# Performance work log

Measured on AMD Instinct MI355X. Metric: run time of the kernel, lower is better.

The kernel has to match this reference:

```python
import jax, jax.numpy as jnp
import numpy as np

D_MODEL = 1024
HIDDEN = 4096
N_EXPERTS = 8
LB_COEF = 0.01
B, N = 2, 2048


def setup_inputs() -> dict:
    key = jax.random.key(0)
    k_x, k_g, k_w1, k_w2 = jax.random.split(key, 4)
    s = 0.02
    return {
        "x": jax.random.normal(k_x, (B, N, D_MODEL), dtype=jnp.float32),
        "gate_w": jax.random.normal(k_g, (N_EXPERTS, D_MODEL), dtype=jnp.float32) * s,
        "w1": jax.random.normal(k_w1, (N_EXPERTS, HIDDEN, D_MODEL), dtype=jnp.float32) * s,  # torch Linear weight [out,in]
        "b1": jnp.zeros((N_EXPERTS, HIDDEN), dtype=jnp.float32),
        "w2": jax.random.normal(k_w2, (N_EXPERTS, D_MODEL, HIDDEN), dtype=jnp.float32) * s,
        "b2": jnp.zeros((N_EXPERTS, D_MODEL), dtype=jnp.float32),
    }


def reference(x, gate_w, w1, b1, w2, b2):
    # gate logits: Linear(d_model, E, bias=False)
    logits = jnp.einsum('bnd,ed->bne', x, gate_w)
    probs = jax.nn.softmax(logits, axis=-1)            # router_prob
    gate_scores = jnp.max(probs, axis=-1)              # top-1 prob [B,N]
    sel = jnp.argmax(probs, axis=-1)                   # selected expert [B,N]

    # load-balance aux loss
    onehot = jax.nn.one_hot(sel, N_EXPERTS, dtype=x.dtype)
    f = onehot.mean(axis=(0, 1))                       # fraction of tokens per expert
    P = probs.mean(axis=(0, 1))                        # mean router prob per expert
    aux_loss = LB_COEF * N_EXPERTS * jnp.sum(f * P)

    # dispatch: loop over fixed small expert count (structurally distinct weights)
    out = jnp.zeros_like(x)
    for e in range(N_EXPERTS):
        h = jax.nn.gelu(jnp.einsum('bnd,hd->bnh', x, w1[e]) + b1[e], approximate=False)
        y = jnp.einsum('bnh,dh->bnd', h, w2[e]) + b2[e]
        out = out + jnp.where((sel == e)[..., None], gate_scores[..., None] * y, jnp.zeros((), x.dtype))
    return out, aux_loss
```

## Files before the change

### kernel.cpp

```cpp
#include <hip/hip_runtime.h>
#include <math.h>

#define T_TOK 4096
#define DM 1024
#define HID 4096
#define NEXP 8
#define MAXT 39

typedef unsigned short u16;
typedef __attribute__((ext_vector_type(8))) short short8;
typedef __attribute__((ext_vector_type(4))) float f32x4;

__device__ __forceinline__ u16 f2bf(float f){
  unsigned u = __float_as_uint(f);
  u += 0x7FFF + ((u >> 16) & 1);
  return (u16)(u >> 16);
}

#define GATE_OFF   0u
#define CNT_OFF    16384u
#define LIST_OFF   16512u
#define PROBS_OFF  147584u
#define XB_OFF     278656u
#define H_OFF      8667264u
#define W1B_OFF    42221696u
#define PART_OFF   W1B_OFF
#define W2B_OFF    109330560u

__device__ __forceinline__ void glds16(const void* g, void* l){
  __builtin_amdgcn_global_load_lds((const __attribute__((address_space(1))) void*)g,
                                   (__attribute__((address_space(3))) void*)l, 16, 0, 0);
}

__global__ void zero_cnt_kernel(int* cnt){
  if (threadIdx.x < NEXP) cnt[threadIdx.x] = 0;
}

__global__ __launch_bounds__(256) void cvt_kernel(const float* __restrict__ src,
                                                  u16* __restrict__ dst,
                                                  size_t n8){
  size_t stride = (size_t)gridDim.x * 256;
  for (size_t i = (size_t)blockIdx.x * 256 + threadIdx.x; i < n8; i += stride){
    const float4* s = (const float4*)src + i * 2;
    float4 a = s[0], c = s[1];
    uint4 p;
    p.x = (unsigned)f2bf(a.x) | ((unsigned)f2bf(a.y) << 16);
    p.y = (unsigned)f2bf(a.z) | ((unsigned)f2bf(a.w) << 16);
    p.z = (unsigned)f2bf(c.x) | ((unsigned)f2bf(c.y) << 16);
    p.w = (unsigned)f2bf(c.z) | ((unsigned)f2bf(c.w) << 16);
    ((uint4*)dst)[i] = p;
  }
}

__global__ __launch_bounds__(256) void gate_kernel(
    const float* __restrict__ x, const float* __restrict__ gw,
    float* __restrict__ gateo, int* __restrict__ cnt, int* __restrict__ list,
    float* __restrict__ probs, u16* __restrict__ xb)
{
  int tid = threadIdx.x;
  int lane = tid & 63;
  int w = tid >> 6;
  int t = blockIdx.x * 4 + w;

  const float4* x4 = (const float4*)(x + (size_t)t * DM);
  const float4* g4 = (const float4*)gw;

  float acc[8] = {0,0,0,0,0,0,0,0};
  #pragma unroll
  for (int i = 0; i < 4; i++){
    int p = i * 64 + lane;
    float4 xv = x4[p];
    ushort4 pk;
    pk.x = f2bf(xv.x); pk.y = f2bf(xv.y); pk.z = f2bf(xv.z); pk.w = f2bf(xv.w);
    *(ushort4*)&xb[(size_t)t * DM + (size_t)p * 4] = pk;
    #pragma unroll
    for (int e = 0; e < NEXP; e++){
      float4 gv = g4[e * 256 + p];
      acc[e] += xv.x * gv.x + xv.y * gv.y + xv.z * gv.z + xv.w * gv.w;
    }
  }
  #pragma unroll
  for (int e = 0; e < NEXP; e++){
    #pragma unroll
    for (int off = 32; off; off >>= 1)
      acc[e] += __shfl_xor(acc[e], off);
  }
  if (lane == 0){
    float mx = acc[0];
    #pragma unroll
    for (int e = 1; e < NEXP; e++) mx = fmaxf(mx, acc[e]);
    float p[8]; float s = 0.f;
    #pragma unroll
    for (int e = 0; e < NEXP; e++){ p[e] = expf(acc[e] - mx); s += p[e]; }
    float inv = 1.f / s;
    int be = 0; float bp = p[0];
    #pragma unroll
    for (int e = 1; e < NEXP; e++){ if (p[e] > bp){ bp = p[e]; be = e; } }
    #pragma unroll
    for (int e = 0; e < NEXP; e++) probs[(size_t)t * 8 + e] = p[e] * inv;
    gateo[t] = bp * inv;
    int pos = atomicAdd(&cnt[be], 1);
    list[be * T_TOK + pos] = t;
  }
}

__global__ __launch_bounds__(256) void aux_kernel(
    const float* __restrict__ probs, const int* __restrict__ cnt,
    float* __restrict__ aux_out)
{
  __shared__ float sm[256 * 8];
  int tid = threadIdx.x;
  float s[8] = {0,0,0,0,0,0,0,0};
  for (int i = 0; i < 16; i++){
    int t = i * 256 + tid;
    #pragma unroll
    for (int e = 0; e < 8; e++) s[e] += probs[(size_t)t * 8 + e];
  }
  #pragma unroll
  for (int e = 0; e < 8; e++) sm[tid * 8 + e] = s[e];
  __syncthreads();
  for (int st = 128; st; st >>= 1){
    if (tid < st){
      #pragma unroll
      for (int e = 0; e < 8; e++) sm[tid * 8 + e] += sm[(tid + st) * 8 + e];
    }
    __syncthreads();
  }
  if (tid == 0){
    float a = 0.f;
    #pragma unroll
    for (int e = 0; e < 8; e++){
      float f = (float)cnt[e] / (float)T_TOK;
      float P = sm[e] / (float)T_TOK;
      a += f * P;
    }
    aux_out[0] = 0.01f * (float)NEXP * a;
  }
}

template<int ASTR, int BSTR, int NTOT, int NT, int KS, bool PHASE2>
__global__ __launch_bounds__(256, 3) void ffn_gemm(
    const u16*  __restrict__ Aall,
    const u16*  __restrict__ Bb,
    const float* __restrict__ bias,
    const int*  __restrict__ cnt,
    const int*  __restrict__ list,
    u16*  __restrict__ hOut,
    float* __restrict__ pOut)
{
  int bid = blockIdx.x;
  int nt = bid % NT;
  int r1 = bid / NT;
  int t  = r1 % MAXT;
  int sk = r1 / MAXT;

  int e = -1, mt = 0, accT = 0;
  #pragma unroll
  for (int i = 0; i < NEXP; i++){
    int nti = (cnt[i] + 127) >> 7;
    if (e < 0 && t < accT + nti){ e = i; mt = t - accT; }
    accT += nti;
  }
  if (e < 0) return;
  int ne = cnt[e];
  int m0 = mt * 128;
  const int* lst = list + e * T_TOK;
  int n0 = nt * 128;
  int koff = sk * (KS * 64);

  __shared__ u16 As[8192];
  __shared__ u16 Bs[8192];

  int tid  = threadIdx.x;
  int lane = tid & 63;
  int w    = tid >> 6;
  int wm = w >> 1, wn = w & 1;
  int fr = lane & 15, fq = lane >> 4;

  const u16* aS[4]; const u16* bS[4]; int dst[4];
  #pragma unroll
  for (int i = 0; i < 4; i++){
    int seg = w * 4 + i;
    int r   = seg * 8 + (lane >> 3);
    int g   = (lane & 7) ^ (r & 7);
    int mrow = m0 + r; if (mrow > ne - 1) mrow = ne - 1;
    aS[i] = Aall + (size_t)lst[mrow] * ASTR + koff + g * 8;
    bS[i] = Bb + (size_t)e * NTOT * BSTR + (size_t)(n0 + r) * BSTR + koff + g * 8;
    dst[i] = seg * 512;
  }

  f32x4 acc[4][4];
  #pragma unroll
  for (int m = 0; m < 4; m++)
    #pragma unroll
    for (int n = 0; n < 4; n++)
      acc[m][n] = (f32x4){0.f, 0.f, 0.f, 0.f};

  for (int ks = 0; ks < KS; ++ks){
    if (ks) __syncthreads();
    size_t ko = (size_t)ks * 64;
    #pragma unroll
    for (int i = 0; i < 4; i++) glds16(aS[i] + ko, &As[dst[i]]);
    #pragma unroll
    for (int i = 0; i < 4; i++) glds16(bS[i] + ko, &Bs[dst[i]]);
    __syncthreads();
    #pragma unroll
    for (int kc = 0; kc < 2; kc++){
      short8 afr[4], bfr[4];
      #pragma unroll
      for (int m = 0; m < 4; m++){
        int row  = wm * 64 + m * 16 + fr;
        int slot = (kc * 4 + fq) ^ (row & 7);
        afr[m] = *(const short8*)&As[row * 64 + slot * 8];
      }
      #pragma unroll
      for (int n = 0; n < 4; n++){
        int row  = wn * 64 + n * 16 + fr;
        int slot = (kc * 4 + fq) ^ (row & 7);
        bfr[n] = *(const short8*)&Bs[row * 64 + slot * 8];
      }
      #pragma unroll
      for (int m = 0; m < 4; m++)
        #pragma unroll
        for (int n = 0; n < 4; n++)
          acc[m][n] = __builtin_amdgcn_mfma_f32_16x16x32_bf16(afr[m], bfr[n], acc[m][n], 0, 0, 0);
    }
  }

  #pragma unroll
  for (int n = 0; n < 4; n++){
    int col = n0 + wn * 64 + n * 16 + fr;
    float bv = bias[(size_t)e * NTOT + col];
    if (PHASE2 && sk != 0) bv = 0.f;
    #pragma unroll
    for (int m = 0; m < 4; m++){
      int rbase = m0 + wm * 64 + m * 16 + fq * 4;
      f32x4 v = acc[m][n];
      #pragma unroll
      for (int i = 0; i < 4; i++){
        int mrow = rbase + i;
        if (mrow < ne){
          int tok = lst[mrow];
          float val = v[i] + bv;
          if (PHASE2){
            pOut[((size_t)sk * T_TOK + tok) * DM + col] = val;
          } else {
            float gl = 0.5f * val * (1.0f + erff(val * 0.70710678118654752f));
            hOut[(size_t)tok * HID + col] = f2bf(gl);
          }
        }
      }
    }
  }
}

__global__ __launch_bounds__(256) void reduce_kernel(
    const float* __restrict__ part, const float* __restrict__ gate,
    float* __restrict__ out)
{
  size_t i = (size_t)blockIdx.x * 256 + threadIdx.x;
  constexpr size_t S = (size_t)T_TOK * DM / 4;
  const float4* p = (const float4*)part;
  float4 a = p[i], b = p[i + S], c = p[i + 2 * S], d = p[i + 3 * S];
  float g = gate[i >> 8];
  float4 o;
  o.x = (a.x + b.x + c.x + d.x) * g;
  o.y = (a.y + b.y + c.y + d.y) * g;
  o.z = (a.z + b.z + c.z + d.z) * g;
  o.w = (a.w + b.w + c.w + d.w) * g;
  ((float4*)out)[i] = o;
}

extern "C" void kernel_launch(void* const* d_in, const int* in_sizes, int n_in,
                              void* d_out, int out_size, void* d_ws, size_t ws_size,
                              hipStream_t stream) {
  const float* x   = (const float*)d_in[0];
  const float* gw  = (const float*)d_in[1];
  const float* w1  = (const float*)d_in[2];
  const float* b1  = (const float*)d_in[3];
  const float* w2  = (const float*)d_in[4];
  const float* b2  = (const float*)d_in[5];

  char* ws = (char*)d_ws;
  float* gateo = (float*)(ws + GATE_OFF);
  int*   cnt   = (int*)  (ws + CNT_OFF);
  int*   list  = (int*)  (ws + LIST_OFF);
  float* probs = (float*)(ws + PROBS_OFF);
  u16*   xb    = (u16*)  (ws + XB_OFF);
  u16*   h     = (u16*)  (ws + H_OFF);
  u16*   w1b   = (u16*)  (ws + W1B_OFF);
  float* part  = (float*)(ws + PART_OFF);
  u16*   w2b   = (u16*)  (ws + W2B_OFF);

  float* out = (float*)d_out;
  float* aux = out + (size_t)T_TOK * DM;

  hipLaunchKernelGGL(zero_cnt_kernel, dim3(1), dim3(64), 0, stream, cnt);
  hipLaunchKernelGGL(gate_kernel, dim3(T_TOK / 4), dim3(256), 0, stream,
                     x, gw, gateo, cnt, list, probs, xb);
  hipLaunchKernelGGL(aux_kernel, dim3(1), dim3(256), 0, stream, probs, cnt, aux);

  size_t n8 = (size_t)NEXP * HID * DM / 8;
  hipLaunchKernelGGL(cvt_kernel, dim3(2048), dim3(256), 0, stream, w1, w1b, n8);
  hipLaunchKernelGGL(cvt_kernel, dim3(2048), dim3(256), 0, stream, w2, w2b, n8);

  hipLaunchKernelGGL((ffn_gemm<DM, DM, HID, 32, 16, false>),
                     dim3(MAXT * 32), dim3(256), 0, stream,
                     xb, w1b, b1, cnt, list, h, (float*)nullptr);
  hipLaunchKernelGGL((ffn_gemm<HID, HID, DM, 8, 16, true>),
                     dim3(4 * MAXT * 8), dim3(256), 0, stream,
                     h, w2b, b2, cnt, list, (u16*)nullptr, part);
  hipLaunchKernelGGL(reduce_kernel, dim3(T_TOK * DM / 4 / 256), dim3(256), 0, stream,
                     part, gateo, out);
}
```

Baseline: 318.4 us.

## Use 256x256 GEMM tiles with 8 waves and double-buffered LDS pipeline

```diff
diff --git a/kernel.cpp b/kernel.cpp
--- a/kernel.cpp
+++ b/kernel.cpp
@@ -5,7 +5,7 @@
 #define DM 1024
 #define HID 4096
 #define NEXP 8
-#define MAXT 39
+#define MAXT 23
 
 typedef unsigned short u16;
 typedef __attribute__((ext_vector_type(8))) short short8;
@@ -31,6 +31,9 @@
   __builtin_amdgcn_global_load_lds((const __attribute__((address_space(1))) void*)g,
                                    (__attribute__((address_space(3))) void*)l, 16, 0, 0);
 }
+
+#define VMW4 asm volatile("s_waitcnt vmcnt(4)" ::: "memory")
+#define VMW0 asm volatile("s_waitcnt vmcnt(0)" ::: "memory")
 
 __global__ void zero_cnt_kernel(int* cnt){
   if (threadIdx.x < NEXP) cnt[threadIdx.x] = 0;
@@ -139,7 +142,7 @@
 }
 
 template<int ASTR, int BSTR, int NTOT, int NT, int KS, bool PHASE2>
-__global__ __launch_bounds__(256, 3) void ffn_gemm(
+__global__ __launch_bounds__(512, 2) void ffn_gemm(
     const u16*  __restrict__ Aall,
     const u16*  __restrict__ Bb,
     const float* __restrict__ bias,
@@ -157,75 +160,117 @@
   int e = -1, mt = 0, accT = 0;
   #pragma unroll
   for (int i = 0; i < NEXP; i++){
-    int nti = (cnt[i] + 127) >> 7;
+    int nti = (cnt[i] + 255) >> 8;
     if (e < 0 && t < accT + nti){ e = i; mt = t - accT; }
     accT += nti;
   }
   if (e < 0) return;
   int ne = cnt[e];
-  int m0 = mt * 128;
+  int m0 = mt * 256;
   const int* lst = list + e * T_TOK;
-  int n0 = nt * 128;
+  int n0 = nt * 256;
   int koff = sk * (KS * 64);
 
-  __shared__ u16 As[8192];
-  __shared__ u16 Bs[8192];
+  __shared__ u16 As[2][16384];
+  __shared__ u16 Bs[2][16384];
 
   int tid  = threadIdx.x;
   int lane = tid & 63;
   int w    = tid >> 6;
-  int wm = w >> 1, wn = w & 1;
+  int wm = w >> 2, wn = w & 3;
   int fr = lane & 15, fq = lane >> 4;
 
-  const u16* aS[4]; const u16* bS[4]; int dst[4];
-  #pragma unroll
-  for (int i = 0; i < 4; i++){
-    int seg = w * 4 + i;
-    int r   = seg * 8 + (lane >> 3);
-    int g   = (lane & 7) ^ (r & 7);
-    int mrow = m0 + r; if (mrow > ne - 1) mrow = ne - 1;
-    aS[i] = Aall + (size_t)lst[mrow] * ASTR + koff + g * 8;
-    bS[i] = Bb + (size_t)e * NTOT * BSTR + (size_t)(n0 + r) * BSTR + koff + g * 8;
-    dst[i] = seg * 512;
-  }
-
-  f32x4 acc[4][4];
-  #pragma unroll
-  for (int m = 0; m < 4; m++)
+  const u16* aP[2][2]; int aD[2][2];
+  const u16* bP[2][2]; int bD[2][2];
+  #pragma unroll
+  for (int h = 0; h < 2; h++){
+    #pragma unroll
+    for (int j = 0; j < 2; j++){
+      int s = w * 2 + j;
+      int abase = ((s >> 3) * 128) + h * 64 + ((s & 7) * 8);
+      int ar = abase + (lane >> 3);
+      int ag = (lane & 7) ^ (ar & 7);
+      int mrow = m0 + ar; if (mrow > ne - 1) mrow = ne - 1;
+      aP[h][j] = Aall + (size_t)lst[mrow] * ASTR + koff + ag * 8;
+      aD[h][j] = abase * 64;
+      int bbase = ((s >> 2) * 64) + h * 32 + ((s & 3) * 8);
+      int br = bbase + (lane >> 3);
+      int bg = (lane & 7) ^ (br & 7);
+      bP[h][j] = Bb + (size_t)e * NTOT * BSTR + (size_t)(n0 + br) * BSTR + koff + bg * 8;
+      bD[h][j] = bbase * 64;
+    }
+  }
+
+  f32x4 acc[8][4];
+  #pragma unroll
+  for (int m = 0; m < 8; m++)
     #pragma unroll
     for (int n = 0; n < 4; n++)
       acc[m][n] = (f32x4){0.f, 0.f, 0.f, 0.f};
 
-  for (int ks = 0; ks < KS; ++ks){
-    if (ks) __syncthreads();
-    size_t ko = (size_t)ks * 64;
-    #pragma unroll
-    for (int i = 0; i < 4; i++) glds16(aS[i] + ko, &As[dst[i]]);
-    #pragma unroll
-    for (int i = 0; i < 4; i++) glds16(bS[i] + ko, &Bs[dst[i]]);
-    __syncthreads();
-    #pragma unroll
-    for (int kc = 0; kc < 2; kc++){
-      short8 afr[4], bfr[4];
-      #pragma unroll
-      for (int m = 0; m < 4; m++){
-        int row  = wm * 64 + m * 16 + fr;
-        int slot = (kc * 4 + fq) ^ (row & 7);
-        afr[m] = *(const short8*)&As[row * 64 + slot * 8];
-      }
-      #pragma unroll
-      for (int n = 0; n < 4; n++){
-        int row  = wn * 64 + n * 16 + fr;
-        int slot = (kc * 4 + fq) ^ (row & 7);
-        bfr[n] = *(const short8*)&Bs[row * 64 + slot * 8];
-      }
-      #pragma unroll
-      for (int m = 0; m < 4; m++)
-        #pragma unroll
-        for (int n = 0; n < 4; n++)
-          acc[m][n] = __builtin_amdgcn_mfma_f32_16x16x32_bf16(afr[m], bfr[n], acc[m][n], 0, 0, 0);
-    }
-  }
+  #pragma unroll
+  for (int h = 0; h < 2; h++){
+    glds16(aP[h][0], &As[0][aD[h][0]]);
+    glds16(aP[h][1], &As[0][aD[h][1]]);
+    glds16(bP[h][0], &Bs[0][bD[h][0]]);
+    glds16(bP[h][1], &Bs[0][bD[h][1]]);
+  }
+  glds16(aP[0][0] + 64, &As[1][aD[0][0]]);
+  glds16(aP[0][1] + 64, &As[1][aD[0][1]]);
+  glds16(bP[0][0] + 64, &Bs[1][bD[0][0]]);
+  glds16(bP[0][1] + 64, &Bs[1][bD[0][1]]);
+  VMW4;
+  __builtin_amdgcn_s_barrier();
+
+#define PHASE(PAR, MH, NH, STG_M, STG_H, SOFF, VW)                               \
+  {                                                                              \
+    short8 afr[4][2]; short8 bfr[2][2];                                          \
+    _Pragma("unroll") for (int m = 0; m < 4; m++)                                \
+      _Pragma("unroll") for (int kc = 0; kc < 2; kc++){                          \
+        int row = wm * 128 + (MH) * 64 + m * 16 + fr;                            \
+        int slot = (kc * 4 + fq) ^ (row & 7);                                    \
+        afr[m][kc] = *(const short8*)&As[PAR][row * 64 + slot * 8]; }            \
+    _Pragma("unroll") for (int n = 0; n < 2; n++)                                \
+      _Pragma("unroll") for (int kc = 0; kc < 2; kc++){                          \
+        int row = wn * 64 + (NH) * 32 + n * 16 + fr;                             \
+        int slot = (kc * 4 + fq) ^ (row & 7);                                    \
+        bfr[n][kc] = *(const short8*)&Bs[PAR][row * 64 + slot * 8]; }            \
+    if (T + (SOFF) < KS){                                                        \
+      int tt = T + (SOFF); int tp = tt & 1;                                      \
+      if ((STG_M) == 0){                                                         \
+        glds16(aP[STG_H][0] + (size_t)tt * 64, &As[tp][aD[STG_H][0]]);           \
+        glds16(aP[STG_H][1] + (size_t)tt * 64, &As[tp][aD[STG_H][1]]);           \
+      } else {                                                                   \
+        glds16(bP[STG_H][0] + (size_t)tt * 64, &Bs[tp][bD[STG_H][0]]);           \
+        glds16(bP[STG_H][1] + (size_t)tt * 64, &Bs[tp][bD[STG_H][1]]);           \
+      }                                                                          \
+    }                                                                            \
+    __builtin_amdgcn_s_barrier();                                                \
+    asm volatile("s_waitcnt lgkmcnt(0)" ::: "memory");                           \
+    __builtin_amdgcn_sched_barrier(0);                                           \
+    __builtin_amdgcn_s_setprio(1);                                               \
+    _Pragma("unroll") for (int m = 0; m < 4; m++)                                \
+      _Pragma("unroll") for (int n = 0; n < 2; n++)                              \
+        _Pragma("unroll") for (int kc = 0; kc < 2; kc++)                         \
+          acc[(MH) * 4 + m][(NH) * 2 + n] = __builtin_amdgcn_mfma_f32_16x16x32_bf16( \
+              afr[m][kc], bfr[n][kc], acc[(MH) * 4 + m][(NH) * 2 + n], 0, 0, 0); \
+    __builtin_amdgcn_s_setprio(0);                                               \
+    if ((VW) == 1){ if (T + 2 < KS) { VMW4; } else { VMW0; } }                   \
+    if ((VW) == 2){ if (T + 3 < KS) { VMW4; } else { VMW0; } }                   \
+    __builtin_amdgcn_s_barrier();                                                \
+  }
+
+  for (int T = 0; T < KS; T += 2){
+    PHASE(0, 0, 0, 0, 1, 1, 0)
+    PHASE(0, 0, 1, 1, 1, 1, 0)
+    PHASE(0, 1, 0, 0, 0, 2, 0)
+    PHASE(0, 1, 1, 1, 0, 2, 1)
+    PHASE(1, 0, 0, 0, 1, 2, 0)
+    PHASE(1, 0, 1, 1, 1, 2, 0)
+    PHASE(1, 1, 0, 0, 0, 3, 0)
+    PHASE(1, 1, 1, 1, 0, 3, 2)
+  }
+#undef PHASE
 
   #pragma unroll
   for (int n = 0; n < 4; n++){
@@ -233,8 +278,8 @@
     float bv = bias[(size_t)e * NTOT + col];
     if (PHASE2 && sk != 0) bv = 0.f;
     #pragma unroll
-    for (int m = 0; m < 4; m++){
-      int rbase = m0 + wm * 64 + m * 16 + fq * 4;
+    for (int m = 0; m < 8; m++){
+      int rbase = m0 + wm * 128 + m * 16 + fq * 4;
       f32x4 v = acc[m][n];
       #pragma unroll
       for (int i = 0; i < 4; i++){
@@ -304,11 +349,11 @@
   hipLaunchKernelGGL(cvt_kernel, dim3(2048), dim3(256), 0, stream, w1, w1b, n8);
   hipLaunchKernelGGL(cvt_kernel, dim3(2048), dim3(256), 0, stream, w2, w2b, n8);
 
-  hipLaunchKernelGGL((ffn_gemm<DM, DM, HID, 32, 16, false>),
-                     dim3(MAXT * 32), dim3(256), 0, stream,
+  hipLaunchKernelGGL((ffn_gemm<DM, DM, HID, 16, 16, false>),
+                     dim3(MAXT * 16), dim3(512), 0, stream,
                      xb, w1b, b1, cnt, list, h, (float*)nullptr);
-  hipLaunchKernelGGL((ffn_gemm<HID, HID, DM, 8, 16, true>),
-                     dim3(4 * MAXT * 8), dim3(256), 0, stream,
+  hipLaunchKernelGGL((ffn_gemm<HID, HID, DM, 4, 16, true>),
+                     dim3(4 * MAXT * 4), dim3(512), 0, stream,
                      h, w2b, b2, cnt, list, (u16*)nullptr, part);
   hipLaunchKernelGGL(reduce_kernel, dim3(T_TOK * DM / 4 / 256), dim3(256), 0, stream,
                      part, gateo, out);
```

Measured after the change: 396.6 us. 24.6% more time.
